# Kernel optimization log

Hardware: AMD Instinct MI355X
Metric: run time of the kernel (lower is better)

The kernel has to match this reference:

```python
import math
import jax, jax.numpy as jnp
import numpy as np

V, D, E, NH, HD, L, FF, RH = 32000, 512, 4, 8, 64, 2, 2048, 256
MPL, MV = 3, 2  # max_path_len, max_visits_per_expert


def _ln(x):
    m = x.mean(-1, keepdims=True)
    v = ((x - m) ** 2).mean(-1, keepdims=True)
    return (x - m) / jnp.sqrt(v + 1e-5)


def _pe(S, d):
    pos = np.arange(S, dtype=np.float32)[:, None]
    div = np.exp(np.arange(0, d, 2, dtype=np.float32) * (-math.log(10000.0) / d))
    pe = np.zeros((S, d), np.float32)
    pe[:, 0::2] = np.sin(pos * div)
    pe[:, 1::2] = np.cos(pos * div)
    return jnp.asarray(pe)[None]  # [1,S,D]


def setup_inputs() -> dict:
    key = jax.random.key(0)
    ks = jax.random.split(key, 24)
    n = lambda k, shp, s=0.02: (jax.random.normal(k, shp, jnp.float32) * s)
    input_ids = jax.random.randint(ks[0], (8, 256), 0, V, dtype=jnp.int32)
    emb = n(ks[1], (V, D)).at[0].set(0.0)  # padding_idx=0
    return {
        "input_ids": input_ids,
        "emb": emb,
        "r_w1": n(ks[2], (RH, D)), "r_b1": jnp.zeros((RH,), jnp.float32),
        "r_w2": n(ks[3], (E + 1, RH)), "r_b2": jnp.zeros((E + 1,), jnp.float32),
        "r_q": jnp.zeros((E + 1,), jnp.float32),
        "in_w": n(ks[4], (E, L, 3 * D, D)), "in_b": jnp.zeros((E, L, 3 * D), jnp.float32),
        "out_w": n(ks[5], (E, L, D, D)), "out_b": jnp.zeros((E, L, D), jnp.float32),
        "gate_w": n(ks[6], (E, L, D, 2 * D)), "gate_b": jnp.zeros((E, L, D), jnp.float32),
        "f_w1": n(ks[7], (E, L, FF, D)), "f_b1": jnp.zeros((E, L, FF), jnp.float32),
        "f_w2": n(ks[8], (E, L, D, FF)), "f_b2": jnp.zeros((E, L, D), jnp.float32),
        "tag": n(ks[9], (E, 1, 1, D), 0.01),
        "lm_w": n(ks[10], (V, D)), "lm_b": jnp.zeros((V,), jnp.float32),
    }


def reference(input_ids, emb, r_w1, r_b1, r_w2, r_b2, r_q,
              in_w, in_b, out_w, out_b, gate_w, gate_b,
              f_w1, f_b1, f_w2, f_b2, tag, lm_w, lm_b):
    B, S = input_ids.shape

    def mha(h, w, b, ow, ob):
        qkv = h @ w.T + b  # [B,S,3D]
        q, k, v = jnp.split(qkv, 3, axis=-1)
        q = q.reshape(B, S, NH, HD); k = k.reshape(B, S, NH, HD); v = v.reshape(B, S, NH, HD)
        att = jax.nn.softmax(jnp.einsum('bqhd,bkhd->bhqk', q, k) / math.sqrt(HD), axis=-1)
        o = jnp.einsum('bhqk,bkhd->bqhd', att, v).reshape(B, S, D)
        return o @ ow.T + ob

    def expert_fwd(p, h):
        iw, ib, ow, ob, gw, gb, w1, b1, w2, b2, tg = p
        for l in range(L):
            z = _ln(h)  # norm1
            ao = mha(z, iw[l], ib[l], ow[l], ob[l])
            g = jax.nn.sigmoid(jnp.concatenate([z, ao], -1) @ gw[l].T + gb[l])
            h = h + _ln(z + g * ao)  # GatedAttention norm + residual
            z2 = _ln(h)  # norm2
            h = h + jax.nn.gelu(z2 @ w1[l].T + b1[l], approximate=False) @ w2[l].T + b2[l]
        return h + tg

    x = emb[input_ids] * math.sqrt(D)
    x = _ln(x + _pe(S, D))  # pos_encoder + input_norm (dropout=eval identity)

    visits = jnp.zeros((B, E), jnp.int32)
    active = jnp.ones((B,), bool)
    ep = (in_w, in_b, out_w, out_b, gate_w, gate_b, f_w1, f_b1, f_w2, f_b2, tag)

    for _ in range(MPL):
        summary = x.mean(axis=1)  # [B,D]
        logits = jax.nn.gelu(summary @ r_w1.T + r_b1, approximate=False) @ r_w2.T + r_b2
        fl = jnp.clip(_ln(logits + r_q[None, :]), -10.0, 10.0)
        ext = jnp.concatenate([visits >= MV, jnp.zeros((B, 1), bool)], axis=-1)
        fl = jnp.where(ext, -jnp.inf, fl)
        action = jnp.argmax(fl, axis=-1)  # E == terminate
        do = active & (action < E)
        all_out = jax.vmap(expert_fwd, in_axes=(0, None))(ep, x)  # [E,B,S,D]
        sel = jax.nn.one_hot(jnp.where(do, action, 0), E, dtype=x.dtype) * do[:, None].astype(x.dtype)
        nx = jnp.einsum('ebsd,be->bsd', all_out, sel)
        x = jnp.where(do[:, None, None], nx, x)
        visits = visits + (sel > 0).astype(jnp.int32)
        active = do

    return _ln(x) @ lm_w.T + lm_b  # final_norm + lm_head  [B,S,V]
```

## Files before the change

kernel.cpp:

```cpp
#include <hip/hip_runtime.h>
#include <hip/hip_bf16.h>
#include <math.h>

#define BB   8
#define SS   256
#define DD   512
#define NHH  8
#define HDD  64
#define EE   4
#define LL   2
#define FFF  2048
#define RHH  256
#define VV   32000
#define MVV  2
#define TOK  (BB*SS)
#define CASTBLK 44672

typedef __attribute__((ext_vector_type(8))) short bf16x8;
typedef __attribute__((ext_vector_type(4))) float f32x4;

__device__ __forceinline__ float wred_sum(float v){
#pragma unroll
  for(int o=32;o;o>>=1) v += __shfl_xor(v,o,64);
  return v;
}
__device__ __forceinline__ float block_sum(float v, float* sh){
  v = wred_sum(v);
  if((threadIdx.x&63)==0) sh[threadIdx.x>>6]=v;
  __syncthreads();
  float t = sh[0]+sh[1]+sh[2]+sh[3];
  __syncthreads();
  return t;
}
__device__ __forceinline__ float gelu_exact(float x){
  return 0.5f*x*(1.f+erff(x*0.70710678118654752f));
}
__device__ __forceinline__ unsigned short bfr(float f){
  union{float f; unsigned u;} c; c.f=f;
  unsigned u = c.u;
  return (unsigned short)((u + 0x7FFFu + ((u>>16)&1u)) >> 16);
}
__device__ __forceinline__ float bff(unsigned short u){
  union{unsigned u; float f;} c; c.u = ((unsigned)u)<<16; return c.f;
}

__global__ void k_preproc(const float* __restrict__ s0,const float* __restrict__ s1,
                          const float* __restrict__ s2,const float* __restrict__ s3,
                          const float* __restrict__ s4,const float* __restrict__ s5,
                          unsigned short* __restrict__ d0,unsigned short* __restrict__ d1,
                          unsigned short* __restrict__ d2,unsigned short* __restrict__ d3,
                          unsigned short* __restrict__ d4,unsigned short* __restrict__ d5,
                          const int* __restrict__ ids, const float* __restrict__ emb,
                          float* __restrict__ x){
  __shared__ float sh[4];
  if(blockIdx.x < CASTBLK){
    long i = (long)blockIdx.x*256 + threadIdx.x;
    const float* s; unsigned short* d; long o;
    if(i < 1572864L){ s=s0; d=d0; o=i; }
    else if(i < 2097152L){ s=s1; d=d1; o=i-1572864L; }
    else if(i < 3145728L){ s=s2; d=d2; o=i-2097152L; }
    else if(i < 5242880L){ s=s3; d=d3; o=i-3145728L; }
    else if(i < 7340032L){ s=s4; d=d4; o=i-5242880L; }
    else { s=s5; d=d5; o=i-7340032L; }
    float4 v = ((const float4*)s)[o];
    ushort4 u; u.x=bfr(v.x); u.y=bfr(v.y); u.z=bfr(v.z); u.w=bfr(v.w);
    ((ushort4*)d)[o] = u;
    return;
  }
  int tok = blockIdx.x - CASTBLK;
  int s = tok & (SS-1);
  int tid = threadIdx.x;
  int id = ids[tok];
  float v[2];
#pragma unroll
  for(int i=0;i<2;i++){
    int d = tid + i*256;
    float e = emb[(size_t)id*DD + d] * 22.627416997969522f;
    int j = d >> 1;
    float freq = expf((float)(2*j) * (-0.0179889460390160f));
    float arg = (float)s * freq;
    v[i] = e + ((d & 1) ? cosf(arg) : sinf(arg));
  }
  float m = block_sum(v[0]+v[1], sh) * (1.f/DD);
  float dd0=v[0]-m, dd1=v[1]-m;
  float var = block_sum(dd0*dd0+dd1*dd1, sh) * (1.f/DD);
  float inv = rsqrtf(var + 1e-5f);
  float* q = x + (size_t)tok*DD;
  q[tid] = dd0*inv; q[tid+256] = dd1*inv;
}

__global__ void k_lnpsum(const float* __restrict__ xin, const float* __restrict__ P0,
                         const float* __restrict__ P1, float* __restrict__ xout,
                         unsigned short* __restrict__ zb,
                         float* __restrict__ psum, const int* __restrict__ dof){
  __shared__ float sh[4];
  int tid = threadIdx.x;
  if(blockIdx.x < TOK){
    int tok = blockIdx.x; int b = tok>>8;
    size_t base = (size_t)tok*DD;
    float a0 = xin[base+tid], a1 = xin[base+tid+256];
    if(P0){
      if(dof[b]){
        a0 += P0[base+tid]     + P1[base+tid];
        a1 += P0[base+tid+256] + P1[base+tid+256];
      }
      xout[base+tid] = a0; xout[base+tid+256] = a1;
    }
    float m = block_sum(a0+a1, sh) * (1.f/DD);
    float d0=a0-m, d1=a1-m;
    float var = block_sum(d0*d0+d1*d1, sh) * (1.f/DD);
    float inv = rsqrtf(var + 1e-5f);
    zb[base+tid] = bfr(d0*inv); zb[base+tid+256] = bfr(d1*inv);
  } else {
    int pb = blockIdx.x - TOK; int b = pb>>4, p = pb&15;
    bool c = (P0 != nullptr) && dof[b];
    float s0=0.f, s1=0.f;
    for(int tt=0; tt<16; tt++){
      size_t r = (size_t)(b*SS + p*16 + tt)*DD;
      float v0 = xin[r+tid], v1 = xin[r+tid+256];
      if(c){ v0 += P0[r+tid]+P1[r+tid]; v1 += P0[r+tid+256]+P1[r+tid+256]; }
      s0 += v0; s1 += v1;
    }
    float* q = psum + (size_t)(b*16+p)*DD;
    q[tid] = s0; q[tid+256] = s1;
  }
}

__global__ void k_router(const float* __restrict__ psum,
                         const float* __restrict__ r_w1, const float* __restrict__ r_b1,
                         const float* __restrict__ r_w2, const float* __restrict__ r_b2,
                         const float* __restrict__ r_q,
                         int* __restrict__ action, int* __restrict__ dof,
                         int* __restrict__ visits, int* __restrict__ active, int step){
  int b = blockIdx.x; int tid = threadIdx.x;
  if(step==0 && tid==0){ active[b]=1; for(int e=0;e<EE;e++) visits[b*EE+e]=0; }
  __shared__ float ssum[DD];
  __shared__ float hid[RHH];
  __shared__ float lg[EE+1];
  float s0=0.f, s1=0.f;
  for(int p=0;p<16;p++){
    const float* q = psum + (size_t)(b*16+p)*DD;
    s0 += q[tid]; s1 += q[tid+256];
  }
  ssum[tid] = s0*(1.f/SS); ssum[tid+256] = s1*(1.f/SS);
  __syncthreads();
  float acc = r_b1[tid];
  const float4* wr4 = (const float4*)(r_w1 + (size_t)tid*DD);
  for(int d4=0; d4<DD/4; d4++){
    float4 wv = wr4[d4];
    float4 sv = *(const float4*)&ssum[d4*4];
    acc += wv.x*sv.x + wv.y*sv.y + wv.z*sv.z + wv.w*sv.w;
  }
  hid[tid] = gelu_exact(acc);
  __syncthreads();
  if(tid < EE+1){
    const float* w2 = r_w2 + (size_t)tid*RHH;
    float a = r_b2[tid] + r_q[tid];
    for(int j=0;j<RHH;j++) a += hid[j]*w2[j];
    lg[tid]=a;
  }
  __syncthreads();
  if(tid==0){
    float m=0.f; for(int k=0;k<EE+1;k++) m+=lg[k]; m *= (1.f/(EE+1));
    float v=0.f; for(int k=0;k<EE+1;k++){float d=lg[k]-m; v+=d*d;} v *= (1.f/(EE+1));
    float inv = rsqrtf(v+1e-5f);
    float best=-1e38f; int bi=0;
    for(int k=0;k<EE+1;k++){
      float fl = (lg[k]-m)*inv;
      fl = fminf(fmaxf(fl,-10.f),10.f);
      if(k<EE && visits[b*EE+k]>=MVV) fl = -1e38f;
      if(fl > best){best=fl; bi=k;}
    }
    int dd = (active[b] && bi<EE) ? 1 : 0;
    action[b]=bi; dof[b]=dd;
    if(dd) visits[b*EE+bi]++;
    active[b]=dd;
  }
}

template<int EPI>
__device__ __forceinline__ void mg64(
    unsigned short* sA, unsigned short* sW,
    const unsigned short* __restrict__ A, int Ald,
    const unsigned short* __restrict__ W, int Wld,
    const float* __restrict__ bias, const float* __restrict__ tagv,
    int N, int K,
    float* __restrict__ Cf, unsigned short* __restrict__ Cb,
    int rowbase, int colbase){
  int t = threadIdx.x;
  int lane = t & 63;
  int w = t >> 6;
  int wcol0 = w*32;
  int sr = t >> 3, ss8 = t & 7;

  f32x4 acc[4][2];
#pragma unroll
  for(int m=0;m<4;m++)
#pragma unroll
    for(int n=0;n<2;n++) acc[m][n] = (f32x4){0.f,0.f,0.f,0.f};

  auto STAGE = [&](int buf, int k0){
    unsigned short* dA = sA + buf*4096;
    unsigned short* dW = sW + buf*8192;
#pragma unroll
    for(int i = 0; i < 2; i++){
      int r  = i*32 + sr;
      int ce = ((ss8<<4) ^ ((r&7)<<4)) >> 1;
      const unsigned short* gp = A + (size_t)(rowbase + r)*Ald + k0 + ce;
      __builtin_amdgcn_global_load_lds((const __attribute__((address_space(1))) void*)gp,
          (__attribute__((address_space(3))) void*)(dA + i*2048 + t*8), 16, 0, 0);
    }
#pragma unroll
    for(int i = 0; i < 4; i++){
      int r  = i*32 + sr;
      int ce = ((ss8<<4) ^ ((r&7)<<4)) >> 1;
      const unsigned short* gw = W + (size_t)(colbase + r)*Wld + k0 + ce;
      __builtin_amdgcn_global_load_lds((const __attribute__((address_space(1))) void*)gw,
          (__attribute__((address_space(3))) void*)(dW + i*2048 + t*8), 16, 0, 0);
    }
  };

  STAGE(0, 0);
  int cur = 0;
  for(int k0 = 0; k0 < K; k0 += 64){
    if(k0 + 64 < K){
      STAGE(cur^1, k0+64);
      asm volatile("s_waitcnt vmcnt(6)" ::: "memory");
    } else {
      asm volatile("s_waitcnt vmcnt(0)" ::: "memory");
    }
    __builtin_amdgcn_s_barrier();
    __builtin_amdgcn_sched_barrier(0);
    const char* bA = (const char*)(sA + cur*4096);
    const char* bW = (const char*)(sW + cur*8192);
#pragma unroll
    for(int ks = 0; ks < 2; ks++){
      bf16x8 af[4], wf[2];
#pragma unroll
      for(int m = 0; m < 4; m++){
        int r = m*16 + (lane & 15);
        af[m] = *(const bf16x8*)(bA + r*128 + (((((lane>>4)<<4)|(ks<<6))) ^ ((r&7)<<4)));
      }
#pragma unroll
      for(int n = 0; n < 2; n++){
        int r = wcol0 + n*16 + (lane & 15);
        wf[n] = *(const bf16x8*)(bW + r*128 + (((((lane>>4)<<4)|(ks<<6))) ^ ((r&7)<<4)));
      }
#pragma unroll
      for(int m = 0; m < 4; m++)
#pragma unroll
        for(int n = 0; n < 2; n++)
          acc[m][n] = __builtin_amdgcn_mfma_f32_16x16x32_bf16(af[m], wf[n], acc[m][n], 0, 0, 0);
    }
    asm volatile("s_waitcnt lgkmcnt(0)" ::: "memory");
    __builtin_amdgcn_s_barrier();
    cur ^= 1;
  }
  int orow0 = rowbase + ((lane >> 4) << 2);
  int ocol0 = colbase + wcol0 + (lane & 15);
#pragma unroll
  for(int m = 0; m < 4; m++){
#pragma unroll
    for(int n = 0; n < 2; n++){
      int col = ocol0 + n*16;
      float addv = (bias ? bias[col] : 0.f) + (tagv ? tagv[col] : 0.f);
#pragma unroll
      for(int j = 0; j < 4; j++){
        int row = orow0 + m*16 + j;
        size_t idx = (size_t)row*N + col;
        float v = acc[m][n][j] + addv;
        if(EPI == 0){ if(Cf) Cf[idx] = v; if(Cb) Cb[idx] = bfr(v); }
        else if(EPI == 1){ Cb[idx] = bfr(gelu_exact(v)); }
        else { Cf[idx] += v; }
      }
    }
  }
}

#define GEMM_LDS __shared__ unsigned short sA[2*64*64]; __shared__ unsigned short sW[2*128*64];

__global__ __launch_bounds__(256)
void k_qkvgate(const unsigned short* __restrict__ z_bf,
               const unsigned short* __restrict__ in_wb, const float* __restrict__ in_b,
               const unsigned short* __restrict__ gate_wb, const float* __restrict__ gate_b,
               unsigned short* __restrict__ qkv_bf, float* __restrict__ gtmp, int l,
               const int* __restrict__ action, const int* __restrict__ dof){
  GEMM_LDS
  int b = blockIdx.x; if(!dof[b]) return;
  size_t o = (size_t)(action[b]*LL + l);
  int rowbase = b*SS + blockIdx.y*64;
  int zz = blockIdx.z;
  if(zz < 12){
    mg64<0>(sA,sW, z_bf,DD, in_wb + o*3*DD*DD, DD, in_b + o*3*DD, nullptr,
            3*DD, DD, nullptr, qkv_bf, rowbase, zz*128);
  } else {
    mg64<0>(sA,sW, z_bf,DD, gate_wb + o*DD*2*DD, 2*DD, gate_b + o*DD, nullptr,
            DD, DD, gtmp, nullptr, rowbase, (zz-12)*128);
  }
}

__global__ __launch_bounds__(256)
void k_out(const unsigned short* __restrict__ attno_bf,
           const unsigned short* __restrict__ out_wb, const float* __restrict__ out_b,
           unsigned short* __restrict__ ao_bf, int l,
           const int* __restrict__ action, const int* __restrict__ dof){
  GEMM_LDS
  int b = blockIdx.x; if(!dof[b]) return;
  size_t o = (size_t)(action[b]*LL + l);
  mg64<0>(sA,sW, attno_bf,DD, out_wb + o*DD*DD, DD, out_b + o*DD, nullptr,
          DD, DD, nullptr, ao_bf, b*SS + blockIdx.y*64, blockIdx.z*128);
}

__global__ __launch_bounds__(256)
void k_gateao(const unsigned short* __restrict__ ao_bf,
              const unsigned short* __restrict__ gate_wb,
              float* __restrict__ gtmp, int l,
              const int* __restrict__ action, const int* __restrict__ dof){
  GEMM_LDS
  int b = blockIdx.x; if(!dof[b]) return;
  size_t o = (size_t)(action[b]*LL + l);
  mg64<2>(sA,sW, ao_bf,DD, gate_wb + o*DD*2*DD + 512, 2*DD, nullptr, nullptr,
          DD, DD, gtmp, nullptr, b*SS + blockIdx.y*64, blockIdx.z*128);
}

__global__ __launch_bounds__(256)
void k_ffn1(const unsigned short* __restrict__ z2_bf,
            const unsigned short* __restrict__ f_w1b, const float* __restrict__ f_b1,
            unsigned short* __restrict__ ffh_bf, int l,
            const int* __restrict__ action, const int* __restrict__ dof){
  GEMM_LDS
  int b = blockIdx.x; if(!dof[b]) return;
  size_t o = (size_t)(action[b]*LL + l);
  mg64<1>(sA,sW, z2_bf,DD, f_w1b + o*FFF*DD, DD, f_b1 + o*FFF, nullptr,
          FFF, DD, nullptr, ffh_bf, b*SS + blockIdx.y*64, blockIdx.z*128);
}

__global__ __launch_bounds__(256)
void k_ffn2(const unsigned short* __restrict__ ffh_bf,
            const unsigned short* __restrict__ f_w2b, const float* __restrict__ f_b2,
            const float* __restrict__ tag,
            float* __restrict__ P0, float* __restrict__ P1, int l,
            const int* __restrict__ action, const int* __restrict__ dof){
  GEMM_LDS
  int b = blockIdx.x; if(!dof[b]) return;
  size_t o = (size_t)(action[b]*LL + l);
  int half = blockIdx.z >> 2, colb = (blockIdx.z & 3)*128;
  const float* bias = half ? nullptr : (f_b2 + o*DD);
  const float* tagv = (half==0 && l==LL-1) ? (tag + (size_t)action[b]*DD) : nullptr;
  mg64<0>(sA,sW, ffh_bf + half*1024, FFF, f_w2b + o*DD*FFF + half*1024, FFF,
          bias, tagv, DD, 1024, half ? P1 : P0, nullptr,
          b*SS + blockIdx.y*64, colb);
}

__global__ __launch_bounds__(256)
void k_attn(const unsigned short* __restrict__ qkv, unsigned short* __restrict__ attno,
            const int* __restrict__ dof){
  int bh = blockIdx.x; int b = bh>>3, h = bh&7;
  if(!dof[b]) return;
  int q0 = blockIdx.y*64;
  __shared__ unsigned short sK[256*64];
  __shared__ unsigned short sVT[64*256];
  int t = threadIdx.x, l = t&63, w = t>>6;
  const unsigned short* qbase = qkv + (size_t)b*SS*1536;

  {
    int sr = t>>3, s8 = t&7;
#pragma unroll
    for(int i=0;i<8;i++){
      int r = i*32 + sr;
      int ce = ((s8<<4) ^ ((r&7)<<4)) >> 1;
      const unsigned short* gp = qbase + (size_t)r*1536 + 512 + h*64 + ce;
      __builtin_amdgcn_global_load_lds((const __attribute__((address_space(1))) void*)gp,
          (__attribute__((address_space(3))) void*)(sK + i*2048 + t*8), 16, 0, 0);
    }
  }
  {
    int kt0 = t>>2, dg = (t&3)*16;
#pragma unroll
    for(int i=0;i<4;i++){
      int kt = i*64 + kt0;
      const unsigned short* gp = qbase + (size_t)kt*1536 + 1024 + h*64 + dg;
      bf16x8 v0 = *(const bf16x8*)gp;
      bf16x8 v1 = *(const bf16x8*)(gp+8);
#pragma unroll
      for(int e=0;e<8;e++){
        int d  = dg+e;
        *(unsigned short*)((char*)sVT + d*512  + ((kt*2) ^ ((d&7)<<4)))  = (unsigned short)v0[e];
        int d2 = dg+8+e;
        *(unsigned short*)((char*)sVT + d2*512 + ((kt*2) ^ ((d2&7)<<4))) = (unsigned short)v1[e];
      }
    }
  }
  bf16x8 qf[2];
  {
    const unsigned short* qrow = qbase + (size_t)(q0 + w*16 + (l&15))*1536 + h*64;
    qf[0] = *(const bf16x8*)(qrow + ((l>>4)<<3));
    qf[1] = *(const bf16x8*)(qrow + ((l>>4)<<3) + 32);
  }
  __syncthreads();

  f32x4 sacc[16];
#pragma unroll
  for(int kb=0;kb<16;kb++) sacc[kb] = (f32x4){0.f,0.f,0.f,0.f};
#pragma unroll
  for(int kb=0;kb<16;kb++){
    int rk = kb*16 + (l&15);
#pragma unroll
    for(int ks=0;ks<2;ks++){
      bf16x8 kf = *(const bf16x8*)((const char*)sK + rk*128 + (((((l>>4)<<4)|(ks<<6))) ^ ((rk&7)<<4)));
      sacc[kb] = __builtin_amdgcn_mfma_f32_16x16x32_bf16(qf[ks], kf, sacc[kb], 0, 0, 0);
    }
  }
  float rden[4];
#pragma unroll
  for(int j=0;j<4;j++){
    float m = -1e38f;
#pragma unroll
    for(int kb=0;kb<16;kb++) m = fmaxf(m, sacc[kb][j]);
#pragma unroll
    for(int o=1;o<16;o<<=1) m = fmaxf(m, __shfl_xor(m,o,64));
    m *= 0.125f;
    float s = 0.f;
#pragma unroll
    for(int kb=0;kb<16;kb++){
      float e = expf(sacc[kb][j]*0.125f - m);
      sacc[kb][j] = e; s += e;
    }
#pragma unroll
    for(int o=1;o<16;o<<=1) s += __shfl_xor(s,o,64);
    rden[j] = 1.f/s;
  }
  __syncthreads();

  char* sP = (char*)sK + w*8192;
#pragma unroll
  for(int kb=0;kb<16;kb++){
    int k = kb*16 + (l&15);
#pragma unroll
    for(int j=0;j<4;j++){
      int qr = ((l>>4)<<2) + j;
      *(unsigned short*)(sP + qr*512 + ((k*2) ^ ((qr&7)<<4))) = bfr(sacc[kb][j]);
    }
  }
  __syncthreads();

  f32x4 oacc[4];
#pragma unroll
  for(int df=0;df<4;df++) oacc[df] = (f32x4){0.f,0.f,0.f,0.f};
#pragma unroll
  for(int kstep=0;kstep<8;kstep++){
    bf16x8 pa = *(const bf16x8*)(sP + (l&15)*512 + ((((kstep<<6)|((l>>4)<<4))) ^ ((l&7)<<4)));
#pragma unroll
    for(int df=0;df<4;df++){
      int d = df*16 + (l&15);
      bf16x8 vb = *(const bf16x8*)((char*)sVT + d*512 + ((((kstep<<6)|((l>>4)<<4))) ^ ((d&7)<<4)));
      oacc[df] = __builtin_amdgcn_mfma_f32_16x16x32_bf16(pa, vb, oacc[df], 0, 0, 0);
    }
  }
  int orow0 = b*SS + q0 + w*16 + ((l>>4)<<2);
#pragma unroll
  for(int df=0;df<4;df++){
    int col = h*64 + df*16 + (l&15);
#pragma unroll
    for(int j=0;j<4;j++)
      attno[(size_t)(orow0+j)*DD + col] = bfr(oacc[df][j]*rden[j]);
  }
}

__global__ void k_gateres_ln(const unsigned short* __restrict__ zb,
                             const unsigned short* __restrict__ aob,
                             const float* __restrict__ g, float* __restrict__ x,
                             unsigned short* __restrict__ z2b, const int* __restrict__ dof){
  int tok = blockIdx.x; if(!dof[tok>>8]) return;
  __shared__ float sh[4];
  int tid=threadIdx.x;
  size_t base=(size_t)tok*DD;
  float zz0=bff(zb[base+tid]),     aa0=bff(aob[base+tid]),     gg0=g[base+tid];
  float zz1=bff(zb[base+tid+256]), aa1=bff(aob[base+tid+256]), gg1=g[base+tid+256];
  float t0 = zz0 + aa0/(1.f+expf(-gg0));
  float t1 = zz1 + aa1/(1.f+expf(-gg1));
  float m = block_sum(t0+t1,sh)*(1.f/DD);
  float d0=t0-m, d1=t1-m;
  float var=block_sum(d0*d0+d1*d1,sh)*(1.f/DD);
  float inv=rsqrtf(var+1e-5f);
  float xn0 = x[base+tid]     + d0*inv;
  float xn1 = x[base+tid+256] + d1*inv;
  x[base+tid] = xn0; x[base+tid+256] = xn1;
  float m2 = block_sum(xn0+xn1,sh)*(1.f/DD);
  float e0=xn0-m2, e1=xn1-m2;
  float var2=block_sum(e0*e0+e1*e1,sh)*(1.f/DD);
  float inv2=rsqrtf(var2+1e-5f);
  z2b[base+tid] = bfr(e0*inv2); z2b[base+tid+256] = bfr(e1*inv2);
}

__global__ __launch_bounds__(512)
void k_lmgemm(const unsigned short* __restrict__ A, const unsigned short* __restrict__ W,
              const float* __restrict__ bias, float* __restrict__ C){
  __shared__ unsigned short sA[2*256*64];
  __shared__ unsigned short sW[2*256*64];
  int t = threadIdx.x, lane = t & 63, w = t >> 6;
  int wr = w >> 2, wc = w & 3;
  int rowbase = blockIdx.y*256, colbase = blockIdx.z*256;
  int sr = t >> 3, ss8 = t & 7;

  f32x4 acc[8][4];
#pragma unroll
  for(int m=0;m<8;m++)
#pragma unroll
    for(int n=0;n<4;n++) acc[m][n] = (f32x4){0.f,0.f,0.f,0.f};

  auto STAGE = [&](int buf, int k0){
    unsigned short* dA = sA + buf*16384;
    unsigned short* dW = sW + buf*16384;
#pragma unroll
    for(int i = 0; i < 4; i++){
      int r  = i*64 + sr;
      int ce = ((ss8<<4) ^ ((r&7)<<4)) >> 1;
      const unsigned short* gp = A + (size_t)(rowbase + r)*DD + k0 + ce;
      __builtin_amdgcn_global_load_lds((const __attribute__((address_space(1))) void*)gp,
          (__attribute__((address_space(3))) void*)(dA + i*4096 + t*8), 16, 0, 0);
      const unsigned short* gw = W + (size_t)(colbase + r)*DD + k0 + ce;
      __builtin_amdgcn_global_load_lds((const __attribute__((address_space(1))) void*)gw,
          (__attribute__((address_space(3))) void*)(dW + i*4096 + t*8), 16, 0, 0);
    }
  };

  STAGE(0, 0);
  int cur = 0;
  for(int k0 = 0; k0 < DD; k0 += 64){
    if(k0 + 64 < DD){
      STAGE(cur^1, k0+64);
      asm volatile("s_waitcnt vmcnt(8)" ::: "memory");
    } else {
      asm volatile("s_waitcnt vmcnt(0)" ::: "memory");
    }
    __builtin_amdgcn_s_barrier();
    __builtin_amdgcn_sched_barrier(0);
    const char* bA = (const char*)(sA + cur*16384);
    const char* bW = (const char*)(sW + cur*16384);
#pragma unroll
    for(int ks = 0; ks < 2; ks++){
      bf16x8 af[8], wf[4];
#pragma unroll
      for(int m = 0; m < 8; m++){
        int r = wr*128 + m*16 + (lane & 15);
        af[m] = *(const bf16x8*)(bA + r*128 + (((((lane>>4)<<4)|(ks<<6))) ^ ((r&7)<<4)));
      }
#pragma unroll
      for(int n = 0; n < 4; n++){
        int r = wc*64 + n*16 + (lane & 15);
        wf[n] = *(const bf16x8*)(bW + r*128 + (((((lane>>4)<<4)|(ks<<6))) ^ ((r&7)<<4)));
      }
#pragma unroll
      for(int m = 0; m < 8; m++)
#pragma unroll
        for(int n = 0; n < 4; n++)
          acc[m][n] = __builtin_amdgcn_mfma_f32_16x16x32_bf16(af[m], wf[n], acc[m][n], 0, 0, 0);
    }
    asm volatile("s_waitcnt lgkmcnt(0)" ::: "memory");
    __builtin_amdgcn_s_barrier();
    cur ^= 1;
  }
  int orow0 = rowbase + wr*128 + ((lane >> 4) << 2);
  int ocol0 = colbase + wc*64 + (lane & 15);
#pragma unroll
  for(int m = 0; m < 8; m++){
#pragma unroll
    for(int n = 0; n < 4; n++){
      int col = ocol0 + n*16;
      float bv = bias[col];
#pragma unroll
      for(int j = 0; j < 4; j++){
        int row = orow0 + m*16 + j;
        C[(size_t)row*VV + col] = acc[m][n][j] + bv;
      }
    }
  }
}

extern "C" void kernel_launch(void* const* d_in, const int* in_sizes, int n_in,
                              void* d_out, int out_size, void* d_ws, size_t ws_size,
                              hipStream_t stream){
  const int*   ids   = (const int*)d_in[0];
  const float* emb   = (const float*)d_in[1];
  const float* r_w1  = (const float*)d_in[2];
  const float* r_b1  = (const float*)d_in[3];
  const float* r_w2  = (const float*)d_in[4];
  const float* r_b2  = (const float*)d_in[5];
  const float* r_q   = (const float*)d_in[6];
  const float* in_w  = (const float*)d_in[7];
  const float* in_b  = (const float*)d_in[8];
  const float* out_w = (const float*)d_in[9];
  const float* out_b = (const float*)d_in[10];
  const float* gate_w= (const float*)d_in[11];
  const float* gate_b= (const float*)d_in[12];
  const float* f_w1  = (const float*)d_in[13];
  const float* f_b1  = (const float*)d_in[14];
  const float* f_w2  = (const float*)d_in[15];
  const float* f_b2  = (const float*)d_in[16];
  const float* tag   = (const float*)d_in[17];
  const float* lm_w  = (const float*)d_in[18];
  const float* lm_b  = (const float*)d_in[19];
  float* out = (float*)d_out;
  float* ws  = (float*)d_ws;

  const size_t M = (size_t)TOK*DD;
  float* x0     = ws;
  float* x1     = ws + 1*M;
  float* gtmp   = ws + 2*M;
  float* P0     = ws + 3*M;
  float* P1     = ws + 4*M;
  float* psum   = ws + 5*M;
  int*   ipool  = (int*)(ws + 5*M + 65536);
  int* action = ipool; int* dof = ipool+BB; int* active = ipool+2*BB; int* visits = ipool+3*BB;

  unsigned short* ub = (unsigned short*)(ws + 5*M + 65536 + 64);
  unsigned short* z_bf     = ub;
  unsigned short* z2_bf    = ub + 1*M;
  unsigned short* attno_bf = ub + 2*M;
  unsigned short* ao_bf    = ub + 3*M;
  unsigned short* qkv_bf   = ub + 4*M;
  unsigned short* ffh_bf   = ub + 7*M;
  unsigned short* wb = ub + 11*M;
  unsigned short* in_wb   = wb;
  unsigned short* out_wb  = in_wb  + (size_t)EE*LL*3*DD*DD;
  unsigned short* gate_wb = out_wb + (size_t)EE*LL*DD*DD;
  unsigned short* f_w1b   = gate_wb+ (size_t)EE*LL*DD*2*DD;
  unsigned short* f_w2b   = f_w1b  + (size_t)EE*LL*FFF*DD;
  unsigned short* lm_wb   = f_w2b  + (size_t)EE*LL*DD*FFF;

  k_preproc<<<CASTBLK+TOK,256,0,stream>>>(in_w,out_w,gate_w,f_w1,f_w2,lm_w,
                                          in_wb,out_wb,gate_wb,f_w1b,f_w2b,lm_wb,
                                          ids, emb, x0);

  float* xc = x0;
  for(int step=0; step<3; step++){
    float* xn = (xc==x0) ? x1 : x0;
    if(step==0)
      k_lnpsum<<<TOK+128,256,0,stream>>>(xc, nullptr, nullptr, xn, z_bf, psum, dof);
    else{
      k_lnpsum<<<TOK+128,256,0,stream>>>(xc, P0, P1, xn, z_bf, psum, dof);
      xc = xn;
    }
    k_router<<<BB,256,0,stream>>>(psum,r_w1,r_b1,r_w2,r_b2,r_q,action,dof,visits,active,step);
    for(int l=0; l<LL; l++){
      if(l==1){
        float* xn2 = (xc==x0) ? x1 : x0;
        k_lnpsum<<<TOK,256,0,stream>>>(xc, P0, P1, xn2, z_bf, nullptr, dof);
        xc = xn2;
      }
      k_qkvgate<<<dim3(BB,4,16),256,0,stream>>>(z_bf, in_wb,in_b, gate_wb,gate_b,
                                                qkv_bf, gtmp, l, action, dof);
      k_attn<<<dim3(BB*NHH,4),256,0,stream>>>(qkv_bf, attno_bf, dof);
      k_out<<<dim3(BB,4,4),256,0,stream>>>(attno_bf, out_wb,out_b, ao_bf, l, action, dof);
      k_gateao<<<dim3(BB,4,4),256,0,stream>>>(ao_bf, gate_wb, gtmp, l, action, dof);
      k_gateres_ln<<<TOK,256,0,stream>>>(z_bf, ao_bf, gtmp, xc, z2_bf, dof);
      k_ffn1<<<dim3(BB,4,16),256,0,stream>>>(z2_bf, f_w1b,f_b1, ffh_bf, l, action, dof);
      k_ffn2<<<dim3(BB,4,8),256,0,stream>>>(ffh_bf, f_w2b,f_b2, tag, P0, P1, l, action, dof);
    }
  }

  {
    float* xn = (xc==x0) ? x1 : x0;
    k_lnpsum<<<TOK,256,0,stream>>>(xc, P0, P1, xn, z_bf, nullptr, dof);
  }
  k_lmgemm<<<dim3(1,8,VV/256),512,0,stream>>>(z_bf, lm_wb, lm_b, out);
}
```

Measured before the change: 731.6 us.

## Precompose gate-half weights with out-projection to fuse out and gate GEMMs

Adds a per-call compose kernel that multiplies the second half of each gate weight by the out-projection weight (and folds the out bias into a gate bias), so the gate contribution from the attention output can be computed directly from the attention output. The former out-projection and gate GEMMs, which ran back to back, become one launch whose blocks split between producing ao and accumulating into gtmp in parallel. This removes a dependent kernel launch per layer step. In exchange it does an extra 8x512x512x512 weight GEMM each call and changes rounding, since the composed weights are stored in bf16.

```diff
diff --git a/kernel.cpp b/kernel.cpp
--- a/kernel.cpp
+++ b/kernel.cpp
@@ -89,6 +89,105 @@
   q[tid] = dd0*inv; q[tid+256] = dd1*inv;
 }
 
+__global__ __launch_bounds__(256)
+void k_compose(const unsigned short* __restrict__ out_wb, const float* __restrict__ out_b,
+               const unsigned short* __restrict__ gate_wb,
+               unsigned short* __restrict__ wext, float* __restrict__ cb){
+  int combo = blockIdx.x;
+  const unsigned short* Wa2 = gate_wb + (size_t)combo*DD*2*DD + 512;
+  const unsigned short* Wo  = out_wb  + (size_t)combo*DD*DD;
+  int c0 = blockIdx.y*64;
+  int t = threadIdx.x;
+  if(blockIdx.z == 4){
+    const float* ob = out_b + (size_t)combo*DD;
+    int c = c0 + (t>>2), q = t&3;
+    float s = 0.f;
+    for(int j=q*128; j<q*128+128; j++) s += bff(Wa2[(size_t)c*1024 + j]) * ob[j];
+    s += __shfl_xor(s,1,64);
+    s += __shfl_xor(s,2,64);
+    if(q==0) cb[(size_t)combo*DD + c] = s;
+    return;
+  }
+  int kb = blockIdx.z*128;
+  __shared__ unsigned short sA[64*64];
+  __shared__ unsigned short sWT[128*64];
+  int lane = t & 63, w = t >> 6;
+  int wcol0 = w*32;
+  f32x4 acc[4][2];
+#pragma unroll
+  for(int m=0;m<4;m++)
+#pragma unroll
+    for(int n=0;n<2;n++) acc[m][n] = (f32x4){0.f,0.f,0.f,0.f};
+
+  for(int j0 = 0; j0 < DD; j0 += 64){
+    {
+      int sr = t>>3, ss8 = t&7;
+#pragma unroll
+      for(int i=0;i<2;i++){
+        int r = i*32 + sr;
+        int ce = ((ss8<<4) ^ ((r&7)<<4)) >> 1;
+        const unsigned short* gp = Wa2 + (size_t)(c0+r)*1024 + j0 + ce;
+        __builtin_amdgcn_global_load_lds((const __attribute__((address_space(1))) void*)gp,
+            (__attribute__((address_space(3))) void*)(sA + i*2048 + t*8), 16, 0, 0);
+      }
+    }
+    {
+      int jr = t>>2, cg = (t&3)*32;
+      const unsigned short* gp = Wo + (size_t)(j0+jr)*DD + kb + cg;
+      bf16x8 v0 = *(const bf16x8*)gp;
+      bf16x8 v1 = *(const bf16x8*)(gp+8);
+      bf16x8 v2 = *(const bf16x8*)(gp+16);
+      bf16x8 v3 = *(const bf16x8*)(gp+24);
+#pragma unroll
+      for(int e=0;e<8;e++){
+        int n0 = cg+e;
+        *(unsigned short*)((char*)sWT + n0*128      + ((jr*2) ^ ((n0&7)<<4)))     = (unsigned short)v0[e];
+        int n1 = cg+8+e;
+        *(unsigned short*)((char*)sWT + n1*128      + ((jr*2) ^ ((n1&7)<<4)))     = (unsigned short)v1[e];
+        int n2 = cg+16+e;
+        *(unsigned short*)((char*)sWT + n2*128      + ((jr*2) ^ ((n2&7)<<4)))     = (unsigned short)v2[e];
+        int n3 = cg+24+e;
+        *(unsigned short*)((char*)sWT + n3*128      + ((jr*2) ^ ((n3&7)<<4)))     = (unsigned short)v3[e];
+      }
+    }
+    asm volatile("s_waitcnt vmcnt(0)" ::: "memory");
+    __syncthreads();
+#pragma unroll
+    for(int ks=0; ks<2; ks++){
+      bf16x8 af[4], wf[2];
+#pragma unroll
+      for(int m=0;m<4;m++){
+        int r = m*16 + (lane & 15);
+        af[m] = *(const bf16x8*)((const char*)sA + r*128 + (((((lane>>4)<<4)|(ks<<6))) ^ ((r&7)<<4)));
+      }
+#pragma unroll
+      for(int n=0;n<2;n++){
+        int r = wcol0 + n*16 + (lane & 15);
+        wf[n] = *(const bf16x8*)((const char*)sWT + r*128 + (((((lane>>4)<<4)|(ks<<6))) ^ ((r&7)<<4)));
+      }
+#pragma unroll
+      for(int m=0;m<4;m++)
+#pragma unroll
+        for(int n=0;n<2;n++)
+          acc[m][n] = __builtin_amdgcn_mfma_f32_16x16x32_bf16(af[m], wf[n], acc[m][n], 0, 0, 0);
+    }
+    __syncthreads();
+  }
+  int orow0 = c0 + ((lane >> 4) << 2);
+  int ocol0 = kb + wcol0 + (lane & 15);
+#pragma unroll
+  for(int m=0;m<4;m++)
+#pragma unroll
+    for(int n=0;n<2;n++){
+      int col = ocol0 + n*16;
+#pragma unroll
+      for(int j=0;j<4;j++){
+        int row = orow0 + m*16 + j;
+        wext[(size_t)combo*DD*DD + (size_t)row*DD + col] = bfr(acc[m][n][j]);
+      }
+    }
+}
+
 __global__ void k_lnpsum(const float* __restrict__ xin, const float* __restrict__ P0,
                          const float* __restrict__ P1, float* __restrict__ xout,
                          unsigned short* __restrict__ zb,
@@ -300,27 +399,23 @@
 }
 
 __global__ __launch_bounds__(256)
-void k_out(const unsigned short* __restrict__ attno_bf,
-           const unsigned short* __restrict__ out_wb, const float* __restrict__ out_b,
-           unsigned short* __restrict__ ao_bf, int l,
-           const int* __restrict__ action, const int* __restrict__ dof){
+void k_outgate(const unsigned short* __restrict__ attno_bf,
+               const unsigned short* __restrict__ out_wb, const float* __restrict__ out_b,
+               const unsigned short* __restrict__ wext, const float* __restrict__ cb,
+               unsigned short* __restrict__ ao_bf, float* __restrict__ gtmp, int l,
+               const int* __restrict__ action, const int* __restrict__ dof){
   GEMM_LDS
   int b = blockIdx.x; if(!dof[b]) return;
   size_t o = (size_t)(action[b]*LL + l);
-  mg64<0>(sA,sW, attno_bf,DD, out_wb + o*DD*DD, DD, out_b + o*DD, nullptr,
-          DD, DD, nullptr, ao_bf, b*SS + blockIdx.y*64, blockIdx.z*128);
-}
-
-__global__ __launch_bounds__(256)
-void k_gateao(const unsigned short* __restrict__ ao_bf,
-              const unsigned short* __restrict__ gate_wb,
-              float* __restrict__ gtmp, int l,
-              const int* __restrict__ action, const int* __restrict__ dof){
-  GEMM_LDS
-  int b = blockIdx.x; if(!dof[b]) return;
-  size_t o = (size_t)(action[b]*LL + l);
-  mg64<2>(sA,sW, ao_bf,DD, gate_wb + o*DD*2*DD + 512, 2*DD, nullptr, nullptr,
-          DD, DD, gtmp, nullptr, b*SS + blockIdx.y*64, blockIdx.z*128);
+  int rowbase = b*SS + blockIdx.y*64;
+  int zz = blockIdx.z;
+  if(zz < 4){
+    mg64<0>(sA,sW, attno_bf,DD, out_wb + o*DD*DD, DD, out_b + o*DD, nullptr,
+            DD, DD, nullptr, ao_bf, rowbase, zz*128);
+  } else {
+    mg64<2>(sA,sW, attno_bf,DD, wext + o*DD*DD, DD, cb + o*DD, nullptr,
+            DD, DD, gtmp, nullptr, rowbase, (zz-4)*128);
+  }
 }
 
 __global__ __launch_bounds__(256)
@@ -611,10 +706,11 @@
   float* P0     = ws + 3*M;
   float* P1     = ws + 4*M;
   float* psum   = ws + 5*M;
-  int*   ipool  = (int*)(ws + 5*M + 65536);
+  float* cbias  = ws + 5*M + 65536;
+  int*   ipool  = (int*)(ws + 5*M + 65536 + 4096);
   int* action = ipool; int* dof = ipool+BB; int* active = ipool+2*BB; int* visits = ipool+3*BB;
 
-  unsigned short* ub = (unsigned short*)(ws + 5*M + 65536 + 64);
+  unsigned short* ub = (unsigned short*)(ws + 5*M + 65536 + 4096 + 64);
   unsigned short* z_bf     = ub;
   unsigned short* z2_bf    = ub + 1*M;
   unsigned short* attno_bf = ub + 2*M;
@@ -628,10 +724,12 @@
   unsigned short* f_w1b   = gate_wb+ (size_t)EE*LL*DD*2*DD;
   unsigned short* f_w2b   = f_w1b  + (size_t)EE*LL*FFF*DD;
   unsigned short* lm_wb   = f_w2b  + (size_t)EE*LL*DD*FFF;
+  unsigned short* wext_b  = lm_wb  + (size_t)VV*DD;
 
   k_preproc<<<CASTBLK+TOK,256,0,stream>>>(in_w,out_w,gate_w,f_w1,f_w2,lm_w,
                                           in_wb,out_wb,gate_wb,f_w1b,f_w2b,lm_wb,
                                           ids, emb, x0);
+  k_compose<<<dim3(8,8,5),256,0,stream>>>(out_wb, out_b, gate_wb, wext_b, cbias);
 
   float* xc = x0;
   for(int step=0; step<3; step++){
@@ -652,8 +750,8 @@
       k_qkvgate<<<dim3(BB,4,16),256,0,stream>>>(z_bf, in_wb,in_b, gate_wb,gate_b,
                                                 qkv_bf, gtmp, l, action, dof);
       k_attn<<<dim3(BB*NHH,4),256,0,stream>>>(qkv_bf, attno_bf, dof);
-      k_out<<<dim3(BB,4,4),256,0,stream>>>(attno_bf, out_wb,out_b, ao_bf, l, action, dof);
-      k_gateao<<<dim3(BB,4,4),256,0,stream>>>(ao_bf, gate_wb, gtmp, l, action, dof);
+      k_outgate<<<dim3(BB,4,8),256,0,stream>>>(attno_bf, out_wb,out_b, wext_b,cbias,
+                                               ao_bf, gtmp, l, action, dof);
       k_gateres_ln<<<TOK,256,0,stream>>>(z_bf, ao_bf, gtmp, xc, z2_bf, dof);
       k_ffn1<<<dim3(BB,4,16),256,0,stream>>>(z2_bf, f_w1b,f_b1, ffh_bf, l, action, dof);
       k_ffn2<<<dim3(BB,4,8),256,0,stream>>>(ffh_bf, f_w2b,f_b2, tag, P0, P1, l, action, dof);
```

New measurement: 730.7 us. About the same (-0.1%).
